# Kernel optimization log

Hardware: AMD Instinct MI355X
Metric: run time of the kernel (lower is better)

## Reference

```python
import jax, jax.numpy as jnp
import numpy as np

B, N, D, H, K = 8, 10000, 128, 4, 256
DH = D // H
M = N // 2


def make_pe(n, d):
    pos = jnp.arange(n, dtype=jnp.float32)[:, None]
    div = jnp.exp(jnp.arange(0, d, 2, dtype=jnp.float32) * (-jnp.log(10000.0) / d))
    ang = pos * div  # [n, d/2]
    pe = jnp.zeros((n, d), dtype=jnp.float32)
    pe = pe.at[:, 0::2].set(jnp.sin(ang))
    pe = pe.at[:, 1::2].set(jnp.cos(ang))
    return pe


def layernorm(z, g, b, eps=1e-5):
    mu = jnp.mean(z, -1, keepdims=True)
    var = jnp.var(z, -1, keepdims=True)
    return (z - mu) / jnp.sqrt(var + eps) * g + b


def setup_inputs():
    key = jax.random.key(0)
    ks = jax.random.split(key, 12)
    def rn(k, shape, scale):
        return jax.random.normal(k, shape, dtype=jnp.float32) * scale
    return {
        "x": rn(ks[0], (B, N), 1.0),
        "emb_w": rn(ks[1], (D, 1), 0.5),
        "emb_b": rn(ks[2], (D,), 0.02),
        "ln1_g": jnp.ones((D,), jnp.float32),
        "ln1_b": jnp.zeros((D,), jnp.float32),
        "wq": rn(ks[3], (D, D), D ** -0.5),
        "wk": rn(ks[4], (D, D), D ** -0.5),
        "wv": rn(ks[5], (D, D), D ** -0.5),
        "proj_k": rn(ks[6], (N, K), N ** -0.5),
        "proj_v": rn(ks[7], (N, K), N ** -0.5),
        "wo": rn(ks[8], (D, D), D ** -0.5),
        "wo_b": jnp.zeros((D,), jnp.float32),
        "ln2_g": jnp.ones((D,), jnp.float32),
        "ln2_b": jnp.zeros((D,), jnp.float32),
        "w1": rn(ks[9], (4 * D, D), D ** -0.5),
        "b1": jnp.zeros((4 * D,), jnp.float32),
        "w2": rn(ks[10], (D, 4 * D), (4 * D) ** -0.5),
        "b2": jnp.zeros((D,), jnp.float32),
        "fc_w": rn(ks[11], (M, N), N ** -0.5),
        "fc_b": jnp.zeros((M,), jnp.float32),
    }


def reference(x, emb_w, emb_b, ln1_g, ln1_b, wq, wk, wv, proj_k, proj_v, wo, wo_b,
              ln2_g, ln2_b, w1, b1, w2, b2, fc_w, fc_b):
    b, n = x.shape
    # Linear embedding of scalar per position: [B,N] -> [B,N,D]
    xe = x[..., None] @ emb_w.T + emb_b
    xe = xe + make_pe(n, D)
    # --- Linformer self-attention block (pre-norm + residual) ---
    hn = layernorm(xe, ln1_g, ln1_b)
    q = hn @ wq.T                                        # [B,N,D]
    k = jnp.einsum('bnd,nk->bkd', hn @ wk.T, proj_k)     # low-rank keys   [B,K,D]
    v = jnp.einsum('bnd,nk->bkd', hn @ wv.T, proj_v)     # low-rank values [B,K,D]
    q = q.reshape(b, n, H, DH).transpose(0, 2, 1, 3)     # [B,H,N,DH]
    k = k.reshape(b, K, H, DH).transpose(0, 2, 1, 3)     # [B,H,K,DH]
    v = v.reshape(b, K, H, DH).transpose(0, 2, 1, 3)
    attn = jax.nn.softmax(jnp.einsum('bhnd,bhkd->bhnk', q, k) * (DH ** -0.5), axis=-1)
    out = jnp.einsum('bhnk,bhkd->bhnd', attn, v).transpose(0, 2, 1, 3).reshape(b, n, D)
    xe = xe + out @ wo.T + wo_b
    # --- FeedForward block (pre-norm + residual, exact GELU) ---
    hn = layernorm(xe, ln2_g, ln2_b)
    xe = xe + (jax.nn.gelu(hn @ w1.T + b1, approximate=False) @ w2.T + b2)
    # fc over seq dim (Linear(N, N//2) applied to [B,D,N]) then sum-pool over D
    y = jnp.einsum('bnd,mn->bdm', xe, fc_w) + fc_b       # [B,D,M]
    return jnp.sum(y, axis=1)                            # [B,M]
```

## Files before the change

### kernel.cpp

```cpp
#include <hip/hip_runtime.h>

constexpr int B_ = 8, N_ = 10000, D_ = 128, H_ = 4, K_ = 256, M_ = 5000, DFF_ = 512;
constexpr int NPAD = 10240;

typedef __attribute__((ext_vector_type(8))) short bf16x8;
typedef __attribute__((ext_vector_type(4))) float f32x4;

__device__ __forceinline__ float bf2f(unsigned short u) {
    unsigned x = ((unsigned)u) << 16; float f; __builtin_memcpy(&f, &x, 4); return f;
}
__device__ __forceinline__ unsigned short f2bf(float f) {
    unsigned x; __builtin_memcpy(&x, &f, 4);
    x = (x + 0x7fffu + ((x >> 16) & 1u)) >> 16;
    return (unsigned short)x;
}
__device__ __forceinline__ unsigned pack2(float a, float b) {
    return (unsigned)f2bf(a) | ((unsigned)f2bf(b) << 16);
}
__device__ __forceinline__ float gelu_tanh(float v) {
    const float z = 0.7978845608028654f * fmaf(0.044715f * v, v * v, v);
    const float e = __expf(2.f * z);
    const float th = fmaf(-2.f, __builtin_amdgcn_rcpf(1.f + e), 1.f);
    return 0.5f * v * (1.f + th);
}

__global__ __launch_bounds__(256) void prep_k(
    const float* __restrict__ wq, const float* __restrict__ wk, const float* __restrict__ wv,
    const float* __restrict__ wo, const float* __restrict__ w1, const float* __restrict__ w2,
    unsigned short* __restrict__ wqb, unsigned short* __restrict__ wkb, unsigned short* __restrict__ wvb,
    unsigned short* __restrict__ wob, unsigned short* __restrict__ w1b, unsigned short* __restrict__ w2b,
    const float* __restrict__ pK, const float* __restrict__ pV, unsigned short* __restrict__ Pt)
{
    __shared__ __align__(16) char lds[16384];
    const int t = threadIdx.x;
    const int flat = blockIdx.x;

    if (flat < 192) {
        const int by = flat / 32, bx = flat % 32;
        const float* s; unsigned short* d; int sz;
        switch (by) {
            case 0: s = wq; d = wqb; sz = 16384; break;
            case 1: s = wk; d = wkb; sz = 16384; break;
            case 2: s = wv; d = wvb; sz = 16384; break;
            case 3: s = wo; d = wob; sz = 16384; break;
            case 4: s = w1; d = w1b; sz = 65536; break;
            default: s = w2; d = w2b; sz = 65536; break;
        }
        const int idx = (bx * 256 + t) * 8;
        if (idx >= sz) return;
        float4 a = *(const float4*)(s + idx);
        float4 b = *(const float4*)(s + idx + 4);
        uint4 p;
        p.x = pack2(a.x, a.y); p.y = pack2(a.z, a.w);
        p.z = pack2(b.x, b.y); p.w = pack2(b.z, b.w);
        *(uint4*)(d + idx) = p;
        return;
    }

    const int f = flat - 192;
    const int bx = f % 160, rest = f / 160;
    const int n0 = bx * 64, k0 = (rest & 1) * 128, which = rest >> 1;
    const float* P = which ? pV : pK;
    {
        const int nl = t >> 2, cc = t & 3;
        const int n = n0 + nl;
        uint4 v[4] = {};
        if (n < N_) {
            const float4* src = (const float4*)(P + (size_t)n * K_ + k0 + cc * 32);
            #pragma unroll
            for (int j = 0; j < 4; ++j) {
                float4 a = src[2 * j], b = src[2 * j + 1];
                uint4 p; p.x = pack2(a.x, a.y); p.y = pack2(a.z, a.w);
                p.z = pack2(b.x, b.y); p.w = pack2(b.z, b.w);
                v[j] = p;
            }
        }
        #pragma unroll
        for (int j = 0; j < 4; ++j) {
            int ch = (cc * 4 + j) ^ (nl & 15);
            *(uint4*)(lds + nl * 256 + ch * 16) = v[j];
        }
    }
    __syncthreads();
    {
        const int eb = t >> 3, nb = t & 7;
        unsigned short r0_[8], r1_[8], r2_[8], r3_[8];
        #pragma unroll
        for (int i = 0; i < 8; ++i) {
            int n = nb * 8 + i;
            int byte_ = n * 256 + (((eb >> 1) ^ (n & 15)) << 4) + ((eb & 1) << 3);
            uint2 dv = *(const uint2*)(lds + byte_);
            r0_[i] = (unsigned short)(dv.x & 0xffff); r1_[i] = (unsigned short)(dv.x >> 16);
            r2_[i] = (unsigned short)(dv.y & 0xffff); r3_[i] = (unsigned short)(dv.y >> 16);
        }
        size_t dbase = ((size_t)which * 256 + k0 + eb * 4) * NPAD + n0 + nb * 8;
        *(uint4*)&Pt[dbase]            = *(uint4*)r0_;
        *(uint4*)&Pt[dbase + NPAD]     = *(uint4*)r1_;
        *(uint4*)&Pt[dbase + 2 * NPAD] = *(uint4*)r2_;
        *(uint4*)&Pt[dbase + 3 * NPAD] = *(uint4*)r3_;
    }
}

__global__ __launch_bounds__(256) void hnt_k(
    const unsigned short* __restrict__ hn, unsigned short* __restrict__ hnT)
{
    __shared__ __align__(16) char lds[16384];
    const int t = threadIdx.x;
    const int n0 = blockIdx.x * 64, b = blockIdx.z;
    {
        const int nl = t >> 2, cc = t & 3;
        const int n = n0 + nl;
        uint4 v[4] = {};
        if (n < N_) {
            const uint4* src = (const uint4*)(hn + ((size_t)(b * N_ + n)) * D_ + cc * 32);
            #pragma unroll
            for (int j = 0; j < 4; ++j) v[j] = src[j];
        }
        #pragma unroll
        for (int j = 0; j < 4; ++j) {
            int ch = (cc * 4 + j) ^ (nl & 15);
            *(uint4*)(lds + nl * 256 + ch * 16) = v[j];
        }
    }
    __syncthreads();
    {
        const int eb = t >> 3, nb = t & 7;
        unsigned short r0_[8], r1_[8], r2_[8], r3_[8];
        #pragma unroll
        for (int i = 0; i < 8; ++i) {
            int n = nb * 8 + i;
            int byte_ = n * 256 + (((eb >> 1) ^ (n & 15)) << 4) + ((eb & 1) << 3);
            uint2 dv = *(const uint2*)(lds + byte_);
            r0_[i] = (unsigned short)(dv.x & 0xffff); r1_[i] = (unsigned short)(dv.x >> 16);
            r2_[i] = (unsigned short)(dv.y & 0xffff); r3_[i] = (unsigned short)(dv.y >> 16);
        }
        size_t dbase = ((size_t)b * 128 + eb * 4) * NPAD + n0 + nb * 8;
        *(uint4*)&hnT[dbase]            = *(uint4*)r0_;
        *(uint4*)&hnT[dbase + NPAD]     = *(uint4*)r1_;
        *(uint4*)&hnT[dbase + 2 * NPAD] = *(uint4*)r2_;
        *(uint4*)&hnT[dbase + 3 * NPAD] = *(uint4*)r3_;
    }
}

__global__ __launch_bounds__(256) void embed_ln_k(
    const float* __restrict__ x, const float* __restrict__ ew, const float* __restrict__ eb,
    const float* __restrict__ g, const float* __restrict__ bb,
    unsigned short* __restrict__ xeb, unsigned short* __restrict__ hnb)
{
    const int r = blockIdx.x * 4 + (threadIdx.x >> 6);
    const int lane = threadIdx.x & 63;
    const int n = r % N_;
    const float xv = x[r];
    const float ang = (float)n * expf((float)lane * -0.14391156829962788f);
    float sv, cv; sincosf(ang, &sv, &cv);
    const int d0 = 2 * lane;
    float e0 = xv * ew[d0]     + eb[d0]     + sv;
    float e1 = xv * ew[d0 + 1] + eb[d0 + 1] + cv;
    float sum = e0 + e1, sq = e0 * e0 + e1 * e1;
    #pragma unroll
    for (int off = 32; off; off >>= 1) { sum += __shfl_xor(sum, off); sq += __shfl_xor(sq, off); }
    const float mu = sum * (1.f / 128.f);
    const float var = sq * (1.f / 128.f) - mu * mu;
    const float rs = rsqrtf(var + 1e-5f);
    const size_t base = (size_t)r * D_ + d0;
    *(unsigned*)&xeb[base] = pack2(e0, e1);
    *(unsigned*)&hnb[base] = pack2((e0 - mu) * rs * g[d0] + bb[d0],
                                   (e1 - mu) * rs * g[d0 + 1] + bb[d0 + 1]);
}

enum { M_Q = 0, M_PROJ = 1, M_SMALL = 2 };

template<int MODE>
__global__ __launch_bounds__(256) void mgemm_k(
    const unsigned short* __restrict__ Abase, const unsigned short* __restrict__ Wbase,
    const unsigned short* __restrict__ Walt,
    float* __restrict__ Cf, unsigned short* __restrict__ Cb)
{
    constexpr int NSTEP = (MODE == M_PROJ) ? 20 : 4;
    constexpr int SA = (MODE == M_PROJ) ? NPAD : 128;
    constexpr int SB = SA;

    __shared__ __align__(16) char lds[16384];

    const int t = threadIdx.x;
    const int bx = blockIdx.x, bz = blockIdx.z;

    const unsigned short* Ag; const unsigned short* Wg; size_t cbase;
    if (MODE == M_PROJ) {
        const int b = (bz >> 4) & 7, chunk = bz & 15, which = bz >> 7;
        Ag = Abase + (size_t)which * 256 * NPAD + (size_t)bx * 128 * NPAD + chunk * 640;
        Wg = Wbase + (size_t)b * 128 * NPAD + chunk * 640;
        cbase = (size_t)bz * 32768 + (size_t)bx * 16384;
    } else if (MODE == M_SMALL) {
        Ag = Abase + (size_t)bz * 2048 * 128 + (size_t)bx * 128 * 128;
        Wg = bz ? Walt : Wbase;
        cbase = (size_t)bz * 262144 + (size_t)bx * 16384;
    } else {
        Ag = Abase + (size_t)bx * 128 * SA;
        Wg = Wbase;
        cbase = (size_t)bx * 128 * 128;
    }

    const int srow = t >> 1, hib = 2 * (t & 1);
    const unsigned short* aptr = Ag + (size_t)srow * SA + hib * 8;
    const unsigned short* wptr = Wg + (size_t)srow * SB + hib * 8;
    const int swz = (srow >> 1) & 3;
    char* la0 = lds + srow * 64 + ((hib ^ swz) << 4);
    char* la1 = lds + srow * 64 + (((hib + 1) ^ swz) << 4);
    char* lw0 = la0 + 8192;
    char* lw1 = la1 + 8192;

    const int w = t >> 6, l = t & 63;
    const int g = l >> 4;
    const int wrow = (w & 1) * 64, wcol = (w >> 1) * 64;
    int offA[4], offW[4];
    #pragma unroll
    for (int mi = 0; mi < 4; ++mi) {
        int ra = wrow + mi * 16 + (l & 15);
        offA[mi] = ra * 64 + (((l >> 4) ^ ((ra >> 1) & 3)) << 4);
        int rw = wcol + mi * 16 + (l & 15);
        offW[mi] = 8192 + rw * 64 + (((l >> 4) ^ ((rw >> 1) & 3)) << 4);
    }

    f32x4 acc[4][4] = {};

    for (int s = 0; s < NSTEP; ++s) {
        uint4 va0 = *(const uint4*)(aptr);
        uint4 va1 = *(const uint4*)(aptr + 8);
        uint4 vw0 = *(const uint4*)(wptr);
        uint4 vw1 = *(const uint4*)(wptr + 8);
        aptr += 32; wptr += 32;
        __syncthreads();
        *(uint4*)la0 = va0; *(uint4*)la1 = va1;
        *(uint4*)lw0 = vw0; *(uint4*)lw1 = vw1;
        __syncthreads();
        bf16x8 af[4], bfr[4];
        #pragma unroll
        for (int mi = 0; mi < 4; ++mi) {
            af[mi] = *(const bf16x8*)(lds + offA[mi]);
            bfr[mi] = *(const bf16x8*)(lds + offW[mi]);
        }
        #pragma unroll
        for (int mi = 0; mi < 4; ++mi)
            #pragma unroll
            for (int ni = 0; ni < 4; ++ni)
                acc[mi][ni] = __builtin_amdgcn_mfma_f32_16x16x32_bf16(af[mi], bfr[ni], acc[mi][ni], 0, 0, 0);
    }

    const int lrb = wrow + (g << 2);
    const int lcb = wcol + (l & 15);
    constexpr bool OBF = (MODE == M_Q || MODE == M_SMALL);
    #pragma unroll
    for (int mi = 0; mi < 4; ++mi) {
        #pragma unroll
        for (int ni = 0; ni < 4; ++ni) {
            const int lc = lcb + ni * 16;
            #pragma unroll
            for (int r = 0; r < 4; ++r) {
                const int lr = lrb + mi * 16 + r;
                const float v = acc[mi][ni][r];
                const size_t ci = cbase + (size_t)lr * 128 + lc;
                if (OBF) Cb[ci] = f2bf(v); else Cf[ci] = v;
            }
        }
    }
}

__global__ __launch_bounds__(256) void reduce_k(
    const float* __restrict__ partials, unsigned short* __restrict__ lowKV)
{
    const int gid = blockIdx.x * 256 + threadIdx.x;
    const int wb = gid >> 15, r = gid & 32767;
    const float* p = partials + (size_t)wb * 16 * 32768 + r;
    float s = 0.f;
    #pragma unroll
    for (int c = 0; c < 16; ++c) s += p[c * 32768];
    lowKV[gid] = f2bf(s);
}

__global__ __launch_bounds__(256) void wo_ffn_k(
    const unsigned short* __restrict__ attn_out, const unsigned short* __restrict__ wob,
    const float* __restrict__ wo_bias, const unsigned short* __restrict__ xeb,
    const float* __restrict__ lng, const float* __restrict__ lnb,
    const unsigned short* __restrict__ w1b, const float* __restrict__ b1,
    const unsigned short* __restrict__ w2b, const float* __restrict__ b2,
    float* __restrict__ st)
{
    __shared__ __align__(16) char lds[34816];
    const int t = threadIdx.x;
    const int w = t >> 6, l = t & 63;
    const int g = l >> 4, ql = l & 15;
    const int r0 = blockIdx.x * 64;
    const int wrow = (w & 1) * 32, wcol = (w >> 1) * 64;
    char* Ald = lds;
    char* Hld = lds + 16384;
    float2* red  = (float2*)(lds + 32768);
    float*  stp  = (float*) (lds + 33792);
    float*  redF = (float*) (lds + 34048);

    {
        const int rr = t >> 2, cc = t & 3;
        #pragma unroll
        for (int j = 0; j < 4; ++j) {
            const int ch = cc * 4 + j;
            const uint4 v = *(const uint4*)(attn_out + (size_t)(r0 + rr) * 128 + ch * 8);
            *(uint4*)(Ald + rr * 256 + ((ch ^ (rr & 15)) << 4)) = v;
        }
    }
    __syncthreads();

    f32x4 wacc[4][2] = {};
    #pragma unroll
    for (int ks = 0; ks < 4; ++ks) {
        const int e0 = ks * 32 + g * 8;
        bf16x8 af[2], wf[4];
        #pragma unroll
        for (int mi = 0; mi < 2; ++mi) {
            const int row = wrow + mi * 16 + ql;
            af[mi] = *(const bf16x8*)(Ald + row * 256 + (((e0 >> 3) ^ (row & 15)) << 4));
        }
        #pragma unroll
        for (int ni = 0; ni < 4; ++ni) {
            const int c = wcol + ni * 16 + ql;
            wf[ni] = *(const bf16x8*)(wob + (size_t)c * 128 + e0);
        }
        #pragma unroll
        for (int ni = 0; ni < 4; ++ni)
            #pragma unroll
            for (int mi = 0; mi < 2; ++mi)
                wacc[ni][mi] = __builtin_amdgcn_mfma_f32_16x16x32_bf16(wf[ni], af[mi], wacc[ni][mi], 0, 0, 0);
    }
    __syncthreads();

    float rsum2[2] = {0.f, 0.f}, rsq2[2] = {0.f, 0.f};
    #pragma unroll
    for (int mi = 0; mi < 2; ++mi) {
        const int row = wrow + mi * 16 + ql;
        #pragma unroll
        for (int ni = 0; ni < 4; ++ni) {
            const int col0 = wcol + ni * 16 + g * 4;
            const float4 wb4 = *(const float4*)&wo_bias[col0];
            const uint2 xr = *(const uint2*)&xeb[(size_t)(r0 + row) * 128 + col0];
            float xv[4];
            xv[0] = bf2f((unsigned short)(xr.x & 0xffff)); xv[1] = bf2f((unsigned short)(xr.x >> 16));
            xv[2] = bf2f((unsigned short)(xr.y & 0xffff)); xv[3] = bf2f((unsigned short)(xr.y >> 16));
            const float wb_[4] = {wb4.x, wb4.y, wb4.z, wb4.w};
            #pragma unroll
            for (int j = 0; j < 4; ++j) {
                const float v = wacc[ni][mi][j] + wb_[j] + xv[j];
                wacc[ni][mi][j] = v;
                rsum2[mi] += v;
                rsq2[mi] += v * v;
            }
        }
    }
    #pragma unroll
    for (int mi = 0; mi < 2; ++mi) {
        rsum2[mi] += __shfl_xor(rsum2[mi], 16); rsum2[mi] += __shfl_xor(rsum2[mi], 32);
        rsq2[mi]  += __shfl_xor(rsq2[mi], 16);  rsq2[mi]  += __shfl_xor(rsq2[mi], 32);
    }
    if (g == 0) {
        #pragma unroll
        for (int mi = 0; mi < 2; ++mi) {
            const int row = wrow + mi * 16 + ql;
            float2 e; e.x = rsum2[mi]; e.y = rsq2[mi];
            red[(w >> 1) * 64 + row] = e;
        }
    }
    __syncthreads();

    #pragma unroll
    for (int mi = 0; mi < 2; ++mi) {
        const int row = wrow + mi * 16 + ql;
        const float2 e0 = red[row], e1 = red[64 + row];
        const float tot = e0.x + e1.x;
        const float mu = tot * (1.f / 128.f);
        const float var = (e0.y + e1.y) * (1.f / 128.f) - mu * mu;
        const float rstd = rsqrtf(var + 1e-5f);
        if (g == 0 && (w >> 1) == 0) stp[row] = tot;
        #pragma unroll
        for (int ni = 0; ni < 4; ++ni) {
            const int col0 = wcol + ni * 16 + g * 4;
            const float4 lg4 = *(const float4*)&lng[col0];
            const float4 lb4 = *(const float4*)&lnb[col0];
            const float lg_[4] = {lg4.x, lg4.y, lg4.z, lg4.w};
            const float lb_[4] = {lb4.x, lb4.y, lb4.z, lb4.w};
            float h_[4];
            #pragma unroll
            for (int j = 0; j < 4; ++j)
                h_[j] = (wacc[ni][mi][j] - mu) * rstd * lg_[j] + lb_[j];
            uint2 pk;
            pk.x = pack2(h_[0], h_[1]);
            pk.y = pack2(h_[2], h_[3]);
            const int chunk = col0 >> 3;
            const int sub = (col0 & 4) << 1;
            *(uint2*)(Ald + row * 256 + ((chunk ^ (row & 15)) << 4) + sub) = pk;
        }
    }
    __syncthreads();

    f32x4 accF[2][4] = {};
    #pragma unroll
    for (int hc = 0; hc < 4; ++hc) {
        f32x4 hacc[4][2] = {};
        #pragma unroll
        for (int ks = 0; ks < 4; ++ks) {
            const int e0 = ks * 32 + g * 8;
            bf16x8 hf[2], wf1[4];
            #pragma unroll
            for (int mi = 0; mi < 2; ++mi) {
                const int row = wrow + mi * 16 + ql;
                hf[mi] = *(const bf16x8*)(Ald + row * 256 + (((e0 >> 3) ^ (row & 15)) << 4));
            }
            #pragma unroll
            for (int ni = 0; ni < 4; ++ni) {
                const int c = hc * 128 + wcol + ni * 16 + ql;
                wf1[ni] = *(const bf16x8*)(w1b + (size_t)c * 128 + e0);
            }
            #pragma unroll
            for (int ni = 0; ni < 4; ++ni)
                #pragma unroll
                for (int mi = 0; mi < 2; ++mi)
                    hacc[ni][mi] = __builtin_amdgcn_mfma_f32_16x16x32_bf16(wf1[ni], hf[mi], hacc[ni][mi], 0, 0, 0);
        }
        #pragma unroll
        for (int ni = 0; ni < 4; ++ni) {
            const int colb = wcol + ni * 16 + g * 4;
            const float4 bb = *(const float4*)&b1[hc * 128 + colb];
            const int chunk = colb >> 3;
            const int sub = (colb & 4) << 1;
            #pragma unroll
            for (int mi = 0; mi < 2; ++mi) {
                const int row = wrow + mi * 16 + ql;
                uint2 pk;
                pk.x = pack2(gelu_tanh(hacc[ni][mi][0] + bb.x), gelu_tanh(hacc[ni][mi][1] + bb.y));
                pk.y = pack2(gelu_tanh(hacc[ni][mi][2] + bb.z), gelu_tanh(hacc[ni][mi][3] + bb.w));
                *(uint2*)(Hld + row * 256 + ((chunk ^ (row & 7)) << 4) + sub) = pk;
            }
        }
        __syncthreads();
        #pragma unroll
        for (int ks = 0; ks < 4; ++ks) {
            const int e0 = ks * 32 + g * 8;
            bf16x8 ah[2], wf2[4];
            #pragma unroll
            for (int mi = 0; mi < 2; ++mi) {
                const int row = wrow + mi * 16 + ql;
                ah[mi] = *(const bf16x8*)(Hld + row * 256 + (((e0 >> 3) ^ (row & 7)) << 4));
            }
            #pragma unroll
            for (int ni = 0; ni < 4; ++ni) {
                const int c = wcol + ni * 16 + ql;
                wf2[ni] = *(const bf16x8*)(w2b + (size_t)c * 512 + hc * 128 + e0);
            }
            #pragma unroll
            for (int mi = 0; mi < 2; ++mi)
                #pragma unroll
                for (int ni = 0; ni < 4; ++ni)
                    accF[mi][ni] = __builtin_amdgcn_mfma_f32_16x16x32_bf16(ah[mi], wf2[ni], accF[mi][ni], 0, 0, 0);
        }
        __syncthreads();
    }

    float b2_c[4];
    #pragma unroll
    for (int ni = 0; ni < 4; ++ni) b2_c[ni] = b2[wcol + ni * 16 + ql];
    float rF[2][4];
    #pragma unroll
    for (int mi = 0; mi < 2; ++mi)
        #pragma unroll
        for (int r = 0; r < 4; ++r) rF[mi][r] = 0.f;
    #pragma unroll
    for (int mi = 0; mi < 2; ++mi)
        #pragma unroll
        for (int ni = 0; ni < 4; ++ni)
            #pragma unroll
            for (int r = 0; r < 4; ++r)
                rF[mi][r] += accF[mi][ni][r] + b2_c[ni];
    #pragma unroll
    for (int mi = 0; mi < 2; ++mi)
        #pragma unroll
        for (int r = 0; r < 4; ++r) {
            float s_ = rF[mi][r];
            #pragma unroll
            for (int off = 1; off < 16; off <<= 1) s_ += __shfl_xor(s_, off);
            rF[mi][r] = s_;
        }
    if (ql == 0) {
        #pragma unroll
        for (int mi = 0; mi < 2; ++mi)
            #pragma unroll
            for (int r = 0; r < 4; ++r)
                redF[(w >> 1) * 64 + wrow + mi * 16 + g * 4 + r] = rF[mi][r];
    }
    __syncthreads();
    if (t < 64) {
        const float total = redF[t] + redF[64 + t] + stp[t];
        const int grow = r0 + t;
        const int bidx = grow / N_;
        const int n = grow - bidx * N_;
        st[(size_t)n * 8 + bidx] = total;
    }
}

__global__ __launch_bounds__(256) void attn_mfma_k(
    const unsigned short* __restrict__ q, const unsigned short* __restrict__ kv,
    unsigned short* __restrict__ outp)
{
    __shared__ __align__(16) char lds[65536];
    const int t = threadIdx.x;
    const int w = t >> 6, l = t & 63;
    const int g = l >> 4, ql = l & 15;
    const int h = blockIdx.y, b = blockIdx.z;
    const int q0 = blockIdx.x * 256;
    const float SC = 0.17677669529663687f;

    #pragma unroll
    for (int i = 0; i < 4; ++i) {
        const int r = (t >> 2) + 64 * i;
        const uint4 v = *(const uint4*)(kv + ((size_t)(b * 256 + r) * 128 + h * 32) + (t & 3) * 8);
        *(uint4*)(lds + r * 64 + (((t & 3) * 16) ^ ((r & 3) << 4))) = v;
    }
    {
        const int kp = t & 127, dhalf = t >> 7;
        const unsigned short* vsrc = kv + 262144 + ((size_t)(b * 256 + 2 * kp) * 128 + h * 32 + 16 * dhalf);
        uint4 a0 = *(const uint4*)(vsrc);
        uint4 a1 = *(const uint4*)(vsrc + 8);
        uint4 c0 = *(const uint4*)(vsrc + 128);
        uint4 c1 = *(const uint4*)(vsrc + 136);
        const unsigned short* pa0 = (const unsigned short*)&a0;
        const unsigned short* pa1 = (const unsigned short*)&a1;
        const unsigned short* pc0 = (const unsigned short*)&c0;
        const unsigned short* pc1 = (const unsigned short*)&c1;
        #pragma unroll
        for (int j = 0; j < 8; ++j) {
            const int row = 16 * dhalf + j;
            unsigned u = (unsigned)pa0[j] | ((unsigned)pc0[j] << 16);
            *(unsigned*)(lds + 16384 + row * 512 + ((4 * kp) ^ ((row & 7) << 4))) = u;
        }
        #pragma unroll
        for (int j = 0; j < 8; ++j) {
            const int row = 16 * dhalf + 8 + j;
            unsigned u = (unsigned)pa1[j] | ((unsigned)pc1[j] << 16);
            *(unsigned*)(lds + 16384 + row * 512 + ((4 * kp) ^ ((row & 7) << 4))) = u;
        }
    }
    bf16x8 qfr[4];
    #pragma unroll
    for (int qf = 0; qf < 4; ++qf) {
        int n = q0 + w * 64 + qf * 16 + ql;
        if (n >= N_) n = N_ - 1;
        qfr[qf] = *(const bf16x8*)(q + ((size_t)(b * N_ + n) * 128 + h * 32 + g * 8));
    }
    __syncthreads();

    char* Pw = lds + 32768 + w * 8192;
    f32x4 oacc[2][4] = {};
    float m_run[4], l_run[4];
    #pragma unroll
    for (int qf = 0; qf < 4; ++qf) { m_run[qf] = -1e30f; l_run[qf] = 0.f; }

    for (int kt = 0; kt < 4; ++kt) {
        const int kb = kt * 64;
        bf16x8 kfr[4];
        #pragma unroll
        for (int kf = 0; kf < 4; ++kf) {
            const int r = kb + kf * 16 + ql;
            kfr[kf] = *(const bf16x8*)(lds + r * 64 + ((g * 16) ^ ((r & 3) << 4)));
        }
        f32x4 s_[4][4];
        #pragma unroll
        for (int kf = 0; kf < 4; ++kf)
            #pragma unroll
            for (int qf = 0; qf < 4; ++qf) {
                f32x4 z = {0.f, 0.f, 0.f, 0.f};
                s_[kf][qf] = __builtin_amdgcn_mfma_f32_16x16x32_bf16(kfr[kf], qfr[qf], z, 0, 0, 0);
            }
        #pragma unroll
        for (int qf = 0; qf < 4; ++qf) {
            float mx = -1e30f;
            #pragma unroll
            for (int kf = 0; kf < 4; ++kf)
                #pragma unroll
                for (int r = 0; r < 4; ++r) mx = fmaxf(mx, s_[kf][qf][r]);
// ... 105 lines not shown
            const float4 wv = *(const float4*)(wrow + nn);
            const float wl[4] = {wv.x, wv.y, wv.z, wv.w};
            #pragma unroll
            for (int j = 0; j < 4; ++j) {
                const float4 sa = *(const float4*)(s_lds + (nn + j) * 8);
                const float4 sb = *(const float4*)(s_lds + (nn + j) * 8 + 4);
                acc[0] = fmaf(wl[j], sa.x, acc[0]); acc[1] = fmaf(wl[j], sa.y, acc[1]);
                acc[2] = fmaf(wl[j], sa.z, acc[2]); acc[3] = fmaf(wl[j], sa.w, acc[3]);
                acc[4] = fmaf(wl[j], sb.x, acc[4]); acc[5] = fmaf(wl[j], sb.y, acc[5]);
                acc[6] = fmaf(wl[j], sb.z, acc[6]); acc[7] = fmaf(wl[j], sb.w, acc[7]);
            }
        }
    }
    #pragma unroll
    for (int j = 0; j < 8; ++j) {
        acc[j] += __shfl_xor(acc[j], 1);
        acc[j] += __shfl_xor(acc[j], 2);
    }
    if (q == 0 && m < M_) {
        float* pb = part + (size_t)blockIdx.y * 40000 + m;
        #pragma unroll
        for (int bb = 0; bb < 8; ++bb) pb[bb * 5000] = acc[bb];
    }
}

__global__ __launch_bounds__(256) void fc_combine_k(
    const float* __restrict__ part, const float* __restrict__ fcb,
    float* __restrict__ out)
{
    const int i = blockIdx.x * 256 + threadIdx.x;
    if (i >= 40000) return;
    float s = 0.f;
    #pragma unroll
    for (int c = 0; c < 5; ++c) s += part[c * 40000 + i];
    const int m = i % 5000;
    out[i] = s + 128.f * fcb[m];
}

extern "C" void kernel_launch(void* const* d_in, const int* in_sizes, int n_in,
                              void* d_out, int out_size, void* d_ws, size_t ws_size,
                              hipStream_t stream)
{
    const float* x      = (const float*)d_in[0];
    const float* emb_w  = (const float*)d_in[1];
    const float* emb_b  = (const float*)d_in[2];
    const float* ln1_g  = (const float*)d_in[3];
    const float* ln1_b  = (const float*)d_in[4];
    const float* wq     = (const float*)d_in[5];
    const float* wk     = (const float*)d_in[6];
    const float* wv     = (const float*)d_in[7];
    const float* projk  = (const float*)d_in[8];
    const float* projv  = (const float*)d_in[9];
    const float* wo     = (const float*)d_in[10];
    const float* wo_b   = (const float*)d_in[11];
    const float* ln2_g  = (const float*)d_in[12];
    const float* ln2_b  = (const float*)d_in[13];
    const float* w1     = (const float*)d_in[14];
    const float* b1     = (const float*)d_in[15];
    const float* w2     = (const float*)d_in[16];
    const float* b2     = (const float*)d_in[17];
    const float* fcw    = (const float*)d_in[18];
    const float* fcb    = (const float*)d_in[19];
    float* out = (float*)d_out;

    char* W = (char*)d_ws;
    unsigned short* xeb      = (unsigned short*)W;
    unsigned short* hnb      = (unsigned short*)(W + 40960000);
    char*           region   = W + 61440000;
    unsigned short* qb       = (unsigned short*)region;
    unsigned short* hnT      = (unsigned short*)(region + 20480000);
    unsigned short* Pt       = (unsigned short*)(region + 41451520);
    float*          partials = (float*)(region + 51937280);
    unsigned short* lowKV    = (unsigned short*)(W + 146931712);
    unsigned short* klowb    = (unsigned short*)(W + 147980288);
    unsigned short* wqb      = (unsigned short*)(W + 150077440);
    unsigned short* wkb      = wqb + 16384;
    unsigned short* wvb      = wkb + 16384;
    unsigned short* wob      = wvb + 16384;
    unsigned short* w1b      = wob + 16384;
    unsigned short* w2b      = w1b + 65536;
    float*          st       = (float*)(W + 150470656);
    float*          fcpart   = (float*)(W + 150790656);

    const size_t BN = (size_t)B_ * N_;

    prep_k<<<832, 256, 0, stream>>>(wq, wk, wv, wo, w1, w2, wqb, wkb, wvb, wob, w1b, w2b,
                                    projk, projv, Pt);
    embed_ln_k<<<BN / 4, 256, 0, stream>>>(x, emb_w, emb_b, ln1_g, ln1_b, xeb, hnb);
    hnt_k<<<dim3(160, 1, 8), 256, 0, stream>>>(hnb, hnT);
    mgemm_k<M_Q><<<dim3(625, 1, 1), 256, 0, stream>>>(hnb, wqb, nullptr, nullptr, qb);
    mgemm_k<M_PROJ><<<dim3(2, 1, 256), 256, 0, stream>>>(Pt, hnT, nullptr, partials, nullptr);
    reduce_k<<<2048, 256, 0, stream>>>(partials, lowKV);
    mgemm_k<M_SMALL><<<dim3(16, 1, 2), 256, 0, stream>>>(lowKV, wkb, wvb, nullptr, klowb);
    attn_mfma_k<<<dim3(40, H_, B_), 256, 0, stream>>>(qb, klowb, hnb);
    wo_ffn_k<<<1250, 256, 0, stream>>>(hnb, wob, wo_b, xeb, ln2_g, ln2_b, w1b, b1, w2b, b2, st);
    fc2_k<<<dim3(79, 5), 256, 0, stream>>>(st, fcw, fcpart);
    fc_combine_k<<<157, 256, 0, stream>>>(fcpart, fcb, out);
}
```

Measured before the change: 319.6 us.

## Merge prep/embed and transpose/Q-GEMM launches; restructure wo_ffn to per-wave rows

Folds the embedding+LayerNorm kernel into the weight-prep kernel, and the hn transpose into the Q projection GEMM, using block-index ranges so each pair becomes one launch. This removes launch overhead and lets independent work overlap. wo_ffn_k is also rewritten so each wave owns 16 full rows across all 128 columns, which drops every __syncthreads and the cross-wave LDS reductions. The cost is more MFMA accumulators per wave and more register pressure, plus branch-divergent mixed-role grids.

```diff
diff --git a/kernel.cpp b/kernel.cpp
--- a/kernel.cpp
+++ b/kernel.cpp
@@ -24,7 +24,10 @@
     return 0.5f * v * (1.f + th);
 }
 
-__global__ __launch_bounds__(256) void prep_k(
+__global__ __launch_bounds__(256) void prep_embed_k(
+    const float* __restrict__ x, const float* __restrict__ ew, const float* __restrict__ eb,
+    const float* __restrict__ g1, const float* __restrict__ bb1,
+    unsigned short* __restrict__ xeb, unsigned short* __restrict__ hnb,
     const float* __restrict__ wq, const float* __restrict__ wk, const float* __restrict__ wv,
     const float* __restrict__ wo, const float* __restrict__ w1, const float* __restrict__ w2,
     unsigned short* __restrict__ wqb, unsigned short* __restrict__ wkb, unsigned short* __restrict__ wvb,
@@ -33,8 +36,32 @@
 {
     __shared__ __align__(16) char lds[16384];
     const int t = threadIdx.x;
-    const int flat = blockIdx.x;
-
+    const int bid = blockIdx.x;
+
+    if (bid < 20000) {
+        const int r = bid * 4 + (t >> 6);
+        const int lane = t & 63;
+        const int n = r % N_;
+        const float xv = x[r];
+        const float ang = (float)n * expf((float)lane * -0.14391156829962788f);
+        float sv, cv; sincosf(ang, &sv, &cv);
+        const int d0 = 2 * lane;
+        float e0 = xv * ew[d0]     + eb[d0]     + sv;
+        float e1 = xv * ew[d0 + 1] + eb[d0 + 1] + cv;
+        float sum = e0 + e1, sq = e0 * e0 + e1 * e1;
+        #pragma unroll
+        for (int off = 32; off; off >>= 1) { sum += __shfl_xor(sum, off); sq += __shfl_xor(sq, off); }
+        const float mu = sum * (1.f / 128.f);
+        const float var = sq * (1.f / 128.f) - mu * mu;
+        const float rs = rsqrtf(var + 1e-5f);
+        const size_t base = (size_t)r * D_ + d0;
+        *(unsigned*)&xeb[base] = pack2(e0, e1);
+        *(unsigned*)&hnb[base] = pack2((e0 - mu) * rs * g1[d0] + bb1[d0],
+                                       (e1 - mu) * rs * g1[d0 + 1] + bb1[d0 + 1]);
+        return;
+    }
+
+    const int flat = bid - 20000;
     if (flat < 192) {
         const int by = flat / 32, bx = flat % 32;
         const float* s; unsigned short* d; int sz;
@@ -83,17 +110,17 @@
     }
     __syncthreads();
     {
-        const int eb = t >> 3, nb = t & 7;
+        const int ebb = t >> 3, nb = t & 7;
         unsigned short r0_[8], r1_[8], r2_[8], r3_[8];
         #pragma unroll
         for (int i = 0; i < 8; ++i) {
             int n = nb * 8 + i;
-            int byte_ = n * 256 + (((eb >> 1) ^ (n & 15)) << 4) + ((eb & 1) << 3);
+            int byte_ = n * 256 + (((ebb >> 1) ^ (n & 15)) << 4) + ((ebb & 1) << 3);
             uint2 dv = *(const uint2*)(lds + byte_);
             r0_[i] = (unsigned short)(dv.x & 0xffff); r1_[i] = (unsigned short)(dv.x >> 16);
             r2_[i] = (unsigned short)(dv.y & 0xffff); r3_[i] = (unsigned short)(dv.y >> 16);
         }
-        size_t dbase = ((size_t)which * 256 + k0 + eb * 4) * NPAD + n0 + nb * 8;
+        size_t dbase = ((size_t)which * 256 + k0 + ebb * 4) * NPAD + n0 + nb * 8;
         *(uint4*)&Pt[dbase]            = *(uint4*)r0_;
         *(uint4*)&Pt[dbase + NPAD]     = *(uint4*)r1_;
         *(uint4*)&Pt[dbase + 2 * NPAD] = *(uint4*)r2_;
@@ -101,74 +128,118 @@
     }
 }
 
-__global__ __launch_bounds__(256) void hnt_k(
-    const unsigned short* __restrict__ hn, unsigned short* __restrict__ hnT)
+__global__ __launch_bounds__(256) void hntq_k(
+    const unsigned short* __restrict__ hn, unsigned short* __restrict__ hnT,
+    const unsigned short* __restrict__ wqb, unsigned short* __restrict__ qb)
 {
     __shared__ __align__(16) char lds[16384];
     const int t = threadIdx.x;
-    const int n0 = blockIdx.x * 64, b = blockIdx.z;
-    {
-        const int nl = t >> 2, cc = t & 3;
-        const int n = n0 + nl;
-        uint4 v[4] = {};
-        if (n < N_) {
-            const uint4* src = (const uint4*)(hn + ((size_t)(b * N_ + n)) * D_ + cc * 32);
-            #pragma unroll
-            for (int j = 0; j < 4; ++j) v[j] = src[j];
-        }
-        #pragma unroll
-        for (int j = 0; j < 4; ++j) {
-            int ch = (cc * 4 + j) ^ (nl & 15);
-            *(uint4*)(lds + nl * 256 + ch * 16) = v[j];
-        }
-    }
-    __syncthreads();
-    {
-        const int eb = t >> 3, nb = t & 7;
-        unsigned short r0_[8], r1_[8], r2_[8], r3_[8];
-        #pragma unroll
-        for (int i = 0; i < 8; ++i) {
-            int n = nb * 8 + i;
-            int byte_ = n * 256 + (((eb >> 1) ^ (n & 15)) << 4) + ((eb & 1) << 3);
-            uint2 dv = *(const uint2*)(lds + byte_);
-            r0_[i] = (unsigned short)(dv.x & 0xffff); r1_[i] = (unsigned short)(dv.x >> 16);
-            r2_[i] = (unsigned short)(dv.y & 0xffff); r3_[i] = (unsigned short)(dv.y >> 16);
-        }
-        size_t dbase = ((size_t)b * 128 + eb * 4) * NPAD + n0 + nb * 8;
-        *(uint4*)&hnT[dbase]            = *(uint4*)r0_;
-        *(uint4*)&hnT[dbase + NPAD]     = *(uint4*)r1_;
-        *(uint4*)&hnT[dbase + 2 * NPAD] = *(uint4*)r2_;
-        *(uint4*)&hnT[dbase + 3 * NPAD] = *(uint4*)r3_;
-    }
-}
-
-__global__ __launch_bounds__(256) void embed_ln_k(
-    const float* __restrict__ x, const float* __restrict__ ew, const float* __restrict__ eb,
-    const float* __restrict__ g, const float* __restrict__ bb,
-    unsigned short* __restrict__ xeb, unsigned short* __restrict__ hnb)
-{
-    const int r = blockIdx.x * 4 + (threadIdx.x >> 6);
-    const int lane = threadIdx.x & 63;
-    const int n = r % N_;
-    const float xv = x[r];
-    const float ang = (float)n * expf((float)lane * -0.14391156829962788f);
-    float sv, cv; sincosf(ang, &sv, &cv);
-    const int d0 = 2 * lane;
-    float e0 = xv * ew[d0]     + eb[d0]     + sv;
-    float e1 = xv * ew[d0 + 1] + eb[d0 + 1] + cv;
-    float sum = e0 + e1, sq = e0 * e0 + e1 * e1;
-    #pragma unroll
-    for (int off = 32; off; off >>= 1) { sum += __shfl_xor(sum, off); sq += __shfl_xor(sq, off); }
-    const float mu = sum * (1.f / 128.f);
-    const float var = sq * (1.f / 128.f) - mu * mu;
-    const float rs = rsqrtf(var + 1e-5f);
-    const size_t base = (size_t)r * D_ + d0;
-    *(unsigned*)&xeb[base] = pack2(e0, e1);
-    *(unsigned*)&hnb[base] = pack2((e0 - mu) * rs * g[d0] + bb[d0],
-                                   (e1 - mu) * rs * g[d0 + 1] + bb[d0 + 1]);
-}
-
-enum { M_Q = 0, M_PROJ = 1, M_SMALL = 2 };
+    const int bid = blockIdx.x;
+
+    if (bid < 1280) {
+        const int n0 = (bid % 160) * 64, b = bid / 160;
+        {
+            const int nl = t >> 2, cc = t & 3;
+            const int n = n0 + nl;
+            uint4 v[4] = {};
+            if (n < N_) {
+                const uint4* src = (const uint4*)(hn + ((size_t)(b * N_ + n)) * D_ + cc * 32);
+                #pragma unroll
+                for (int j = 0; j < 4; ++j) v[j] = src[j];
+            }
+            #pragma unroll
+            for (int j = 0; j < 4; ++j) {
+                int ch = (cc * 4 + j) ^ (nl & 15);
+                *(uint4*)(lds + nl * 256 + ch * 16) = v[j];
+            }
+        }
+        __syncthreads();
+        {
+            const int ebb = t >> 3, nb = t & 7;
+            unsigned short r0_[8], r1_[8], r2_[8], r3_[8];
+            #pragma unroll
+            for (int i = 0; i < 8; ++i) {
+                int n = nb * 8 + i;
+                int byte_ = n * 256 + (((ebb >> 1) ^ (n & 15)) << 4) + ((ebb & 1) << 3);
+                uint2 dv = *(const uint2*)(lds + byte_);
+                r0_[i] = (unsigned short)(dv.x & 0xffff); r1_[i] = (unsigned short)(dv.x >> 16);
+                r2_[i] = (unsigned short)(dv.y & 0xffff); r3_[i] = (unsigned short)(dv.y >> 16);
+            }
+            size_t dbase = ((size_t)b * 128 + ebb * 4) * NPAD + n0 + nb * 8;
+            *(uint4*)&hnT[dbase]            = *(uint4*)r0_;
+            *(uint4*)&hnT[dbase + NPAD]     = *(uint4*)r1_;
+            *(uint4*)&hnT[dbase + 2 * NPAD] = *(uint4*)r2_;
+            *(uint4*)&hnT[dbase + 3 * NPAD] = *(uint4*)r3_;
+        }
+        return;
+    }
+
+    const int bx = bid - 1280;
+    const unsigned short* Ag = hn + (size_t)bx * 128 * 128;
+    const unsigned short* Wg = wqb;
+    const size_t cbase = (size_t)bx * 16384;
+
+    const int srow = t >> 1, hib = 2 * (t & 1);
+    const unsigned short* aptr = Ag + (size_t)srow * 128 + hib * 8;
+    const unsigned short* wptr = Wg + (size_t)srow * 128 + hib * 8;
+    const int swz = (srow >> 1) & 3;
+    char* la0 = lds + srow * 64 + ((hib ^ swz) << 4);
+    char* la1 = lds + srow * 64 + (((hib + 1) ^ swz) << 4);
+    char* lw0 = la0 + 8192;
+    char* lw1 = la1 + 8192;
+
+    const int w = t >> 6, l = t & 63;
+    const int g = l >> 4;
+    const int wrow = (w & 1) * 64, wcol = (w >> 1) * 64;
+    int offA[4], offW[4];
+    #pragma unroll
+    for (int mi = 0; mi < 4; ++mi) {
+        int ra = wrow + mi * 16 + (l & 15);
+        offA[mi] = ra * 64 + (((l >> 4) ^ ((ra >> 1) & 3)) << 4);
+        int rw = wcol + mi * 16 + (l & 15);
+        offW[mi] = 8192 + rw * 64 + (((l >> 4) ^ ((rw >> 1) & 3)) << 4);
+    }
+
+    f32x4 acc[4][4] = {};
+    for (int s = 0; s < 4; ++s) {
+        uint4 va0 = *(const uint4*)(aptr);
+        uint4 va1 = *(const uint4*)(aptr + 8);
+        uint4 vw0 = *(const uint4*)(wptr);
+        uint4 vw1 = *(const uint4*)(wptr + 8);
+        aptr += 32; wptr += 32;
+        __syncthreads();
+        *(uint4*)la0 = va0; *(uint4*)la1 = va1;
+        *(uint4*)lw0 = vw0; *(uint4*)lw1 = vw1;
+        __syncthreads();
+        bf16x8 af[4], bfr[4];
+        #pragma unroll
+        for (int mi = 0; mi < 4; ++mi) {
+            af[mi] = *(const bf16x8*)(lds + offA[mi]);
+            bfr[mi] = *(const bf16x8*)(lds + offW[mi]);
+        }
+        #pragma unroll
+        for (int mi = 0; mi < 4; ++mi)
+            #pragma unroll
+            for (int ni = 0; ni < 4; ++ni)
+                acc[mi][ni] = __builtin_amdgcn_mfma_f32_16x16x32_bf16(af[mi], bfr[ni], acc[mi][ni], 0, 0, 0);
+    }
+
+    const int lrb = wrow + (g << 2);
+    const int lcb = wcol + (l & 15);
+    #pragma unroll
+    for (int mi = 0; mi < 4; ++mi)
+        #pragma unroll
+        for (int ni = 0; ni < 4; ++ni) {
+            const int lc = lcb + ni * 16;
+            #pragma unroll
+            for (int r = 0; r < 4; ++r) {
+                const int lr = lrb + mi * 16 + r;
+                qb[cbase + (size_t)lr * 128 + lc] = f2bf(acc[mi][ni][r]);
+            }
+        }
+}
+
+enum { M_PROJ = 1, M_SMALL = 2 };
 
 template<int MODE>
 __global__ __launch_bounds__(256) void mgemm_k(
@@ -191,14 +262,10 @@
         Ag = Abase + (size_t)which * 256 * NPAD + (size_t)bx * 128 * NPAD + chunk * 640;
         Wg = Wbase + (size_t)b * 128 * NPAD + chunk * 640;
         cbase = (size_t)bz * 32768 + (size_t)bx * 16384;
-    } else if (MODE == M_SMALL) {
+    } else {
         Ag = Abase + (size_t)bz * 2048 * 128 + (size_t)bx * 128 * 128;
         Wg = bz ? Walt : Wbase;
         cbase = (size_t)bz * 262144 + (size_t)bx * 16384;
-    } else {
-        Ag = Abase + (size_t)bx * 128 * SA;
-        Wg = Wbase;
-        cbase = (size_t)bx * 128 * 128;
     }
 
     const int srow = t >> 1, hib = 2 * (t & 1);
@@ -249,7 +316,6 @@
 
     const int lrb = wrow + (g << 2);
     const int lcb = wcol + (l & 15);
-    constexpr bool OBF = (MODE == M_Q || MODE == M_SMALL);
     #pragma unroll
     for (int mi = 0; mi < 4; ++mi) {
         #pragma unroll
@@ -260,7 +326,7 @@
                 const int lr = lrb + mi * 16 + r;
                 const float v = acc[mi][ni][r];
                 const size_t ci = cbase + (size_t)lr * 128 + lc;
-                if (OBF) Cb[ci] = f2bf(v); else Cf[ci] = v;
+                if (MODE == M_SMALL) Cb[ci] = f2bf(v); else Cf[ci] = v;
             }
         }
     }
@@ -286,220 +352,142 @@
     const unsigned short* __restrict__ w2b, const float* __restrict__ b2,
     float* __restrict__ st)
 {
-    __shared__ __align__(16) char lds[34816];
+    __shared__ __align__(16) char lds[32768];
     const int t = threadIdx.x;
     const int w = t >> 6, l = t & 63;
     const int g = l >> 4, ql = l & 15;
-    const int r0 = blockIdx.x * 64;
-    const int wrow = (w & 1) * 32, wcol = (w >> 1) * 64;
-    char* Ald = lds;
-    char* Hld = lds + 16384;
-    float2* red  = (float2*)(lds + 32768);
-    float*  stp  = (float*) (lds + 33792);
-    float*  redF = (float*) (lds + 34048);
+    const int r0 = blockIdx.x * 64 + w * 16;
+    char* SA = lds + w * 4096;
+    char* SH = lds + 16384 + w * 4096;
 
     {
-        const int rr = t >> 2, cc = t & 3;
+        const int rr = l >> 2, cc = l & 3;
         #pragma unroll
         for (int j = 0; j < 4; ++j) {
             const int ch = cc * 4 + j;
             const uint4 v = *(const uint4*)(attn_out + (size_t)(r0 + rr) * 128 + ch * 8);
-            *(uint4*)(Ald + rr * 256 + ((ch ^ (rr & 15)) << 4)) = v;
-        }
-    }
-    __syncthreads();
-
-    f32x4 wacc[4][2] = {};
+            *(uint4*)(SA + rr * 256 + ((ch ^ rr) << 4)) = v;
+        }
+    }
+
+    f32x4 wacc[8] = {};
     #pragma unroll
     for (int ks = 0; ks < 4; ++ks) {
         const int e0 = ks * 32 + g * 8;
-        bf16x8 af[2], wf[4];
-        #pragma unroll
-        for (int mi = 0; mi < 2; ++mi) {
-            const int row = wrow + mi * 16 + ql;
-            af[mi] = *(const bf16x8*)(Ald + row * 256 + (((e0 >> 3) ^ (row & 15)) << 4));
-        }
-        #pragma unroll
-        for (int ni = 0; ni < 4; ++ni) {
-            const int c = wcol + ni * 16 + ql;
-            wf[ni] = *(const bf16x8*)(wob + (size_t)c * 128 + e0);
-        }
-        #pragma unroll
-        for (int ni = 0; ni < 4; ++ni)
-            #pragma unroll
-            for (int mi = 0; mi < 2; ++mi)
-                wacc[ni][mi] = __builtin_amdgcn_mfma_f32_16x16x32_bf16(wf[ni], af[mi], wacc[ni][mi], 0, 0, 0);
-    }
-    __syncthreads();
-
-    float rsum2[2] = {0.f, 0.f}, rsq2[2] = {0.f, 0.f};
-    #pragma unroll
-    for (int mi = 0; mi < 2; ++mi) {
-        const int row = wrow + mi * 16 + ql;
-        #pragma unroll
-        for (int ni = 0; ni < 4; ++ni) {
-            const int col0 = wcol + ni * 16 + g * 4;
-            const float4 wb4 = *(const float4*)&wo_bias[col0];
-            const uint2 xr = *(const uint2*)&xeb[(size_t)(r0 + row) * 128 + col0];
-            float xv[4];
-            xv[0] = bf2f((unsigned short)(xr.x & 0xffff)); xv[1] = bf2f((unsigned short)(xr.x >> 16));
-            xv[2] = bf2f((unsigned short)(xr.y & 0xffff)); xv[3] = bf2f((unsigned short)(xr.y >> 16));
-            const float wb_[4] = {wb4.x, wb4.y, wb4.z, wb4.w};
-            #pragma unroll
-            for (int j = 0; j < 4; ++j) {
-                const float v = wacc[ni][mi][j] + wb_[j] + xv[j];
-                wacc[ni][mi][j] = v;
-                rsum2[mi] += v;
-                rsq2[mi] += v * v;
-            }
-        }
-    }
-    #pragma unroll
-    for (int mi = 0; mi < 2; ++mi) {
-        rsum2[mi] += __shfl_xor(rsum2[mi], 16); rsum2[mi] += __shfl_xor(rsum2[mi], 32);
-        rsq2[mi]  += __shfl_xor(rsq2[mi], 16);  rsq2[mi]  += __shfl_xor(rsq2[mi], 32);
-    }
-    if (g == 0) {
-        #pragma unroll
-        for (int mi = 0; mi < 2; ++mi) {
-            const int row = wrow + mi * 16 + ql;
-            float2 e; e.x = rsum2[mi]; e.y = rsq2[mi];
-            red[(w >> 1) * 64 + row] = e;
-        }
-    }
-    __syncthreads();
-
-    #pragma unroll
-    for (int mi = 0; mi < 2; ++mi) {
-        const int row = wrow + mi * 16 + ql;
-        const float2 e0 = red[row], e1 = red[64 + row];
-        const float tot = e0.x + e1.x;
-        const float mu = tot * (1.f / 128.f);
-        const float var = (e0.y + e1.y) * (1.f / 128.f) - mu * mu;
-        const float rstd = rsqrtf(var + 1e-5f);
-        if (g == 0 && (w >> 1) == 0) stp[row] = tot;
-        #pragma unroll
-        for (int ni = 0; ni < 4; ++ni) {
-            const int col0 = wcol + ni * 16 + g * 4;
-            const float4 lg4 = *(const float4*)&lng[col0];
-            const float4 lb4 = *(const float4*)&lnb[col0];
-            const float lg_[4] = {lg4.x, lg4.y, lg4.z, lg4.w};
-            const float lb_[4] = {lb4.x, lb4.y, lb4.z, lb4.w};
-            float h_[4];
-            #pragma unroll
-            for (int j = 0; j < 4; ++j)
-                h_[j] = (wacc[ni][mi][j] - mu) * rstd * lg_[j] + lb_[j];
-            uint2 pk;
-            pk.x = pack2(h_[0], h_[1]);
-            pk.y = pack2(h_[2], h_[3]);
-            const int chunk = col0 >> 3;
-            const int sub = (col0 & 4) << 1;
-            *(uint2*)(Ald + row * 256 + ((chunk ^ (row & 15)) << 4) + sub) = pk;
-        }
-    }
-    __syncthreads();
-
-    f32x4 accF[2][4] = {};
+        const bf16x8 af = *(const bf16x8*)(SA + ql * 256 + (((e0 >> 3) ^ ql) << 4));
+        #pragma unroll
+        for (int ni = 0; ni < 8; ++ni) {
+            const bf16x8 wf = *(const bf16x8*)(wob + (size_t)(ni * 16 + ql) * 128 + e0);
+            wacc[ni] = __builtin_amdgcn_mfma_f32_16x16x32_bf16(wf, af, wacc[ni], 0, 0, 0);
+        }
+    }
+
+    float rsum = 0.f, rsq = 0.f;
+    #pragma unroll
+    for (int ni = 0; ni < 8; ++ni) {
+        const int col0 = ni * 16 + g * 4;
+        const float4 wb4 = *(const float4*)&wo_bias[col0];
+        const uint2 xr = *(const uint2*)&xeb[(size_t)(r0 + ql) * 128 + col0];
+        float xv[4];
+        xv[0] = bf2f((unsigned short)(xr.x & 0xffff)); xv[1] = bf2f((unsigned short)(xr.x >> 16));
+        xv[2] = bf2f((unsigned short)(xr.y & 0xffff)); xv[3] = bf2f((unsigned short)(xr.y >> 16));
+        const float wb_[4] = {wb4.x, wb4.y, wb4.z, wb4.w};
+        #pragma unroll
+        for (int j = 0; j < 4; ++j) {
+            const float v = wacc[ni][j] + wb_[j] + xv[j];
+            wacc[ni][j] = v;
+            rsum += v;
+            rsq += v * v;
+        }
+    }
+    rsum += __shfl_xor(rsum, 16); rsum += __shfl_xor(rsum, 32);
+    rsq  += __shfl_xor(rsq, 16);  rsq  += __shfl_xor(rsq, 32);
+    const float tot = rsum;
+    const float mu = tot * (1.f / 128.f);
+    const float var = rsq * (1.f / 128.f) - mu * mu;
+    const float rstd = rsqrtf(var + 1e-5f);
+
+    #pragma unroll
+    for (int ni = 0; ni < 8; ++ni) {
+        const int col0 = ni * 16 + g * 4;
+        const float4 lg4 = *(const float4*)&lng[col0];
+        const float4 lb4 = *(const float4*)&lnb[col0];
+        const float lg_[4] = {lg4.x, lg4.y, lg4.z, lg4.w};
+        const float lb_[4] = {lb4.x, lb4.y, lb4.z, lb4.w};
+        float h_[4];
+        #pragma unroll
+        for (int j = 0; j < 4; ++j)
+            h_[j] = (wacc[ni][j] - mu) * rstd * lg_[j] + lb_[j];
+        uint2 pk;
+        pk.x = pack2(h_[0], h_[1]);
+        pk.y = pack2(h_[2], h_[3]);
+        const int chunk = col0 >> 3;
+        const int sub = (col0 & 4) << 1;
+        *(uint2*)(SA + ql * 256 + ((chunk ^ ql) << 4) + sub) = pk;
+    }
+
+    f32x4 accF[8] = {};
     #pragma unroll
     for (int hc = 0; hc < 4; ++hc) {
-        f32x4 hacc[4][2] = {};
+        f32x4 hacc[8] = {};
         #pragma unroll
         for (int ks = 0; ks < 4; ++ks) {
             const int e0 = ks * 32 + g * 8;
-            bf16x8 hf[2], wf1[4];
-            #pragma unroll
-            for (int mi = 0; mi < 2; ++mi) {
-                const int row = wrow + mi * 16 + ql;
-                hf[mi] = *(const bf16x8*)(Ald + row * 256 + (((e0 >> 3) ^ (row & 15)) << 4));
-            }
-            #pragma unroll
-            for (int ni = 0; ni < 4; ++ni) {
-                const int c = hc * 128 + wcol + ni * 16 + ql;
-                wf1[ni] = *(const bf16x8*)(w1b + (size_t)c * 128 + e0);
-            }
-            #pragma unroll
-            for (int ni = 0; ni < 4; ++ni)
-                #pragma unroll
-                for (int mi = 0; mi < 2; ++mi)
-                    hacc[ni][mi] = __builtin_amdgcn_mfma_f32_16x16x32_bf16(wf1[ni], hf[mi], hacc[ni][mi], 0, 0, 0);
-        }
-        #pragma unroll
-        for (int ni = 0; ni < 4; ++ni) {
-            const int colb = wcol + ni * 16 + g * 4;
+            const bf16x8 hf = *(const bf16x8*)(SA + ql * 256 + (((e0 >> 3) ^ ql) << 4));
+            #pragma unroll
+            for (int ni = 0; ni < 8; ++ni) {
+                const bf16x8 wf1 = *(const bf16x8*)(w1b + (size_t)(hc * 128 + ni * 16 + ql) * 128 + e0);
+                hacc[ni] = __builtin_amdgcn_mfma_f32_16x16x32_bf16(wf1, hf, hacc[ni], 0, 0, 0);
+            }
+        }
+        #pragma unroll
+        for (int ni = 0; ni < 8; ++ni) {
+            const int colb = ni * 16 + g * 4;
             const float4 bb = *(const float4*)&b1[hc * 128 + colb];
-            const int chunk = colb >> 3;
+            uint2 pk;
+            pk.x = pack2(gelu_tanh(hacc[ni][0] + bb.x), gelu_tanh(hacc[ni][1] + bb.y));
+            pk.y = pack2(gelu_tanh(hacc[ni][2] + bb.z), gelu_tanh(hacc[ni][3] + bb.w));
+            const int chb = colb >> 3;
             const int sub = (colb & 4) << 1;
-            #pragma unroll
-            for (int mi = 0; mi < 2; ++mi) {
-                const int row = wrow + mi * 16 + ql;
-                uint2 pk;
-                pk.x = pack2(gelu_tanh(hacc[ni][mi][0] + bb.x), gelu_tanh(hacc[ni][mi][1] + bb.y));
-                pk.y = pack2(gelu_tanh(hacc[ni][mi][2] + bb.z), gelu_tanh(hacc[ni][mi][3] + bb.w));
-                *(uint2*)(Hld + row * 256 + ((chunk ^ (row & 7)) << 4) + sub) = pk;
-            }
-        }
-        __syncthreads();
+            *(uint2*)(SH + ql * 256 + ((chb ^ ql) << 4) + sub) = pk;
+        }
         #pragma unroll
         for (int ks = 0; ks < 4; ++ks) {
             const int e0 = ks * 32 + g * 8;
-            bf16x8 ah[2], wf2[4];
-            #pragma unroll
-            for (int mi = 0; mi < 2; ++mi) {
-                const int row = wrow + mi * 16 + ql;
-                ah[mi] = *(const bf16x8*)(Hld + row * 256 + (((e0 >> 3) ^ (row & 7)) << 4));
-            }
-            #pragma unroll
-            for (int ni = 0; ni < 4; ++ni) {
-                const int c = wcol + ni * 16 + ql;
-                wf2[ni] = *(const bf16x8*)(w2b + (size_t)c * 512 + hc * 128 + e0);
-            }
-            #pragma unroll
-            for (int mi = 0; mi < 2; ++mi)
-                #pragma unroll
-                for (int ni = 0; ni < 4; ++ni)
-                    accF[mi][ni] = __builtin_amdgcn_mfma_f32_16x16x32_bf16(ah[mi], wf2[ni], accF[mi][ni], 0, 0, 0);
-        }
-        __syncthreads();
-    }
-
-    float b2_c[4];
-    #pragma unroll
-    for (int ni = 0; ni < 4; ++ni) b2_c[ni] = b2[wcol + ni * 16 + ql];
-    float rF[2][4];
-    #pragma unroll
-    for (int mi = 0; mi < 2; ++mi)
-        #pragma unroll
-        for (int r = 0; r < 4; ++r) rF[mi][r] = 0.f;
-    #pragma unroll
-    for (int mi = 0; mi < 2; ++mi)
-        #pragma unroll
-        for (int ni = 0; ni < 4; ++ni)
-            #pragma unroll
-            for (int r = 0; r < 4; ++r)
-                rF[mi][r] += accF[mi][ni][r] + b2_c[ni];
-    #pragma unroll
-    for (int mi = 0; mi < 2; ++mi)
+            const bf16x8 ah = *(const bf16x8*)(SH + ql * 256 + (((e0 >> 3) ^ ql) << 4));
+            #pragma unroll
+            for (int ni = 0; ni < 8; ++ni) {
+                const bf16x8 wf2 = *(const bf16x8*)(w2b + (size_t)(ni * 16 + ql) * 512 + hc * 128 + e0);
+                accF[ni] = __builtin_amdgcn_mfma_f32_16x16x32_bf16(ah, wf2, accF[ni], 0, 0, 0);
+            }
+        }
+    }
+
+    float rF[4] = {0.f, 0.f, 0.f, 0.f};
+    #pragma unroll
+    for (int ni = 0; ni < 8; ++ni) {
+        const float b2c = b2[ni * 16 + ql];
+        #pragma unroll
+        for (int r = 0; r < 4; ++r) rF[r] += accF[ni][r] + b2c;
+    }
+    #pragma unroll
+    for (int r = 0; r < 4; ++r) {
+        rF[r] += __shfl_xor(rF[r], 1);
+        rF[r] += __shfl_xor(rF[r], 2);
+        rF[r] += __shfl_xor(rF[r], 4);
+        rF[r] += __shfl_xor(rF[r], 8);
+    }
+    float totr[4];
+    #pragma unroll
+    for (int r = 0; r < 4; ++r) totr[r] = __shfl(tot, g * 4 + r);
+    if (ql == 0) {
         #pragma unroll
         for (int r = 0; r < 4; ++r) {
-            float s_ = rF[mi][r];
-            #pragma unroll
-            for (int off = 1; off < 16; off <<= 1) s_ += __shfl_xor(s_, off);
-            rF[mi][r] = s_;
-        }
-    if (ql == 0) {
-        #pragma unroll
-        for (int mi = 0; mi < 2; ++mi)
-            #pragma unroll
-            for (int r = 0; r < 4; ++r)
-                redF[(w >> 1) * 64 + wrow + mi * 16 + g * 4 + r] = rF[mi][r];
-    }
-    __syncthreads();
-    if (t < 64) {
-        const float total = redF[t] + redF[64 + t] + stp[t];
-        const int grow = r0 + t;
-        const int bidx = grow / N_;
-        const int n = grow - bidx * N_;
-        st[(size_t)n * 8 + bidx] = total;
+            const int grow = r0 + g * 4 + r;
+            const int bidx = grow / N_;
+            const int n = grow - bidx * N_;
+            st[(size_t)n * 8 + bidx] = rF[r] + totr[r];
+        }
     }
 }
 
@@ -771,13 +759,11 @@
     float*          st       = (float*)(W + 150470656);
     float*          fcpart   = (float*)(W + 150790656);
 
-    const size_t BN = (size_t)B_ * N_;
-
-    prep_k<<<832, 256, 0, stream>>>(wq, wk, wv, wo, w1, w2, wqb, wkb, wvb, wob, w1b, w2b,
-                                    projk, projv, Pt);
-    embed_ln_k<<<BN / 4, 256, 0, stream>>>(x, emb_w, emb_b, ln1_g, ln1_b, xeb, hnb);
-    hnt_k<<<dim3(160, 1, 8), 256, 0, stream>>>(hnb, hnT);
-    mgemm_k<M_Q><<<dim3(625, 1, 1), 256, 0, stream>>>(hnb, wqb, nullptr, nullptr, qb);
+    prep_embed_k<<<20832, 256, 0, stream>>>(x, emb_w, emb_b, ln1_g, ln1_b, xeb, hnb,
+                                            wq, wk, wv, wo, w1, w2,
+                                            wqb, wkb, wvb, wob, w1b, w2b,
+                                            projk, projv, Pt);
+    hntq_k<<<1905, 256, 0, stream>>>(hnb, hnT, wqb, qb);
     mgemm_k<M_PROJ><<<dim3(2, 1, 256), 256, 0, stream>>>(Pt, hnT, nullptr, partials, nullptr);
     reduce_k<<<2048, 256, 0, stream>>>(partials, lowKV);
     mgemm_k<M_SMALL><<<dim3(16, 1, 2), 256, 0, stream>>>(lowKV, wkb, wvb, nullptr, klowb);
```

Result: slower. 387.0 us (+21.1%).
